# Optimization experiments

Measured on AMD Instinct MI355X. Metric: run time of the kernel, lower is better.

Reference implementation:

```python
import jax, jax.numpy as jnp
import numpy as np

N_NODES = 10000
N_EDGES = 640000
D_FEAT = 128
EPS = 1e-12  # F.normalize default eps


def setup_inputs() -> dict:
    key = jax.random.key(0)
    k1, k2, k3 = jax.random.split(key, 3)
    x = jax.random.normal(k1, (N_NODES, D_FEAT), dtype=jnp.float32)
    edge = jax.random.randint(k2, (3, N_EDGES), 0, N_NODES, dtype=jnp.int64)
    edge_weight = jax.random.uniform(k3, (N_EDGES,), dtype=jnp.float32)
    return {"x": x, "edge": edge, "edge_weight": edge_weight}


def reference(x, edge, edge_weight):
    edge_j = edge[0]  # source nodes
    edge_i = edge[2]  # target nodes
    n = x.shape[0]
    # degree of each target node (scatter_add of edge weights)
    deg = jax.ops.segment_sum(edge_weight, edge_i, num_segments=n)
    # normalized edge weights: w_e = ew_e / deg[target(e)]
    w = edge_weight / deg[edge_i]
    # SpMM: out[i] = sum_{e: target=i} w_e * x[source(e)]
    msg = x[edge_j] * w[:, None]           # [E, D]
    out = jax.ops.segment_sum(msg, edge_i, num_segments=n)  # [N, D]
    out = jax.nn.relu(out)
    # row-wise L2 normalize (F.normalize: x / max(||x||, eps))
    norm = jnp.sqrt(jnp.sum(out * out, axis=1, keepdims=True))
    return out / jnp.maximum(norm, EPS)
```

## Files before the change

kernel.cpp:

```cpp
#include <hip/hip_runtime.h>
#include <hip/hip_fp16.h>
#include <math.h>

#define D_FEAT 128
#define EPS 1e-12f
#define TGRP 40
#define NBUCK_PAD 256
#define NBLK 250
#define CAP_CB 40
#define SLOTS_PB (NBLK * CAP_CB)
#define LCAP 3584


__device__ inline float2 h2_to_f2(unsigned int u) {
    __half2 h = *reinterpret_cast<__half2*>(&u);
    return __half22float2(h);
}

__device__ inline float w12_to_f(unsigned int p) {
    return __half2float(__ushort_as_half((unsigned short)((p & 0xfffu) << 4)));
}

__global__ __launch_bounds__(1024)
void build_kernel(const int* __restrict__ edge_i,
                  const int* __restrict__ edge_j,
                  const float* __restrict__ ew,
                  const float* __restrict__ x,
                  unsigned int* __restrict__ xh,
                  unsigned char* __restrict__ cntcb,
                  unsigned int* __restrict__ payload,
                  int E, int total4, int nbuck) {
    __shared__ unsigned int hc[NBUCK_PAD];
    const int c   = blockIdx.x;
    const int tid = threadIdx.x;
    const int EPB = E / NBLK;

    if (tid < NBUCK_PAD) hc[tid] = 0;
    __syncthreads();

    for (int i = c * 1024 + tid; i < total4; i += NBLK * 1024) {
        float4 v = ((const float4*)x)[i];
        __half2 h01 = __floats2half2_rn(v.x, v.y);
        __half2 h23 = __floats2half2_rn(v.z, v.w);
        uint2 o;
        o.x = *reinterpret_cast<unsigned int*>(&h01);
        o.y = *reinterpret_cast<unsigned int*>(&h23);
        ((uint2*)xh)[i] = o;
    }

    const int e0 = c * EPB;
    for (int k = tid; k < EPB; k += 1024) {
        int e = e0 + k;
        int t = edge_i[e];
        int bkt  = t / TGRP;
        int tloc = t - bkt * TGRP;
        unsigned int r = atomicAdd(&hc[bkt], 1u);
        if (r < CAP_CB) {
            unsigned int hw = (unsigned int)__half_as_ushort(__float2half(ew[e]));
            unsigned int w12 = (hw + 8u) >> 4;
            payload[(size_t)bkt * SLOTS_PB + c * CAP_CB + r] =
                ((unsigned int)edge_j[e] << 18) | ((unsigned int)tloc << 12) | w12;
        }
    }
    __syncthreads();

    if (tid < nbuck) {
        unsigned int v = hc[tid];
        cntcb[(size_t)tid * NBUCK_PAD + c] =
            (unsigned char)(v > CAP_CB ? CAP_CB : v);
    }
}

__global__ __launch_bounds__(1024)
void sort_gather_kernel(const unsigned char* __restrict__ cntcb,
                        const unsigned int* __restrict__ payload,
                        const unsigned int* __restrict__ xh,
                        float* __restrict__ out, int n) {
    __shared__ unsigned char cnt_c[NBLK];
    __shared__ unsigned int  stmp[256];
    __shared__ unsigned int  chunkbase[NBLK + 1];
    __shared__ unsigned int  cnt40[TGRP];
    __shared__ unsigned int  base40[TGRP + 1];
    __shared__ unsigned int  ssw0[LCAP];
    __shared__ unsigned int  ssw[LCAP];
    const int b    = blockIdx.x;
    const int tid  = threadIdx.x;
    const int wv   = tid >> 6;
    const int lane = tid & 63;
    const int g    = lane >> 4;
    const int l16  = lane & 15;

    if (tid < NBLK) cnt_c[tid] = cntcb[(size_t)b * NBUCK_PAD + tid];
    if (tid < TGRP) cnt40[tid] = 0;
    __syncthreads();

    unsigned int v0 = 0;
    if (tid < 256) {
        v0 = (tid < NBLK) ? (unsigned int)cnt_c[tid] : 0u;
        stmp[tid] = v0;
    }
    __syncthreads();
    for (int off = 1; off < 256; off <<= 1) {
        unsigned int u = 0;
        if (tid < 256 && tid >= off) u = stmp[tid - off];
        __syncthreads();
        if (tid < 256) stmp[tid] += u;
        __syncthreads();
    }
    if (tid < NBLK) chunkbase[tid] = stmp[tid] - v0;
    if (tid == 255) chunkbase[NBLK] = stmp[255];
    __syncthreads();

    const unsigned int* __restrict__ pb = payload + (size_t)b * SLOTS_PB;
    for (int s = tid; s < SLOTS_PB; s += 1024) {
        unsigned int p = pb[s];
        int c = s / CAP_CB;
        int k = s - c * CAP_CB;
        if (k < (int)cnt_c[c]) {
            unsigned int pos = chunkbase[c] + (unsigned int)k;
            if (pos < LCAP) ssw0[pos] = p;
        }
    }
    __syncthreads();

    unsigned int M = chunkbase[NBLK];
    if (M > LCAP) M = LCAP;

    unsigned int pcar[4]; unsigned int dcar[4]; int ncar = 0;
    for (unsigned int i = tid; i < M; i += 1024) {
        unsigned int p = ssw0[i];
        unsigned int tloc = (p >> 12) & 63u;
        unsigned int r = atomicAdd(&cnt40[tloc], 1u);
        pcar[ncar] = p;
        dcar[ncar] = (tloc << 16) | (r & 0xffffu);
        ++ncar;
    }
    __syncthreads();

    if (tid == 0) {
        unsigned int run = 0;
        #pragma unroll
        for (int t = 0; t < TGRP; ++t) { base40[t] = run; run += cnt40[t]; }
        base40[TGRP] = run;
    }
    __syncthreads();

    for (int q = 0; q < ncar; ++q) {
        unsigned int d = dcar[q];
        unsigned int pos = base40[d >> 16] + (d & 0xffffu);
        if (pos < LCAP) ssw[pos] = pcar[q];
    }
    __syncthreads();

    const uint4* __restrict__ xr = (const uint4*)xh;
    for (int tl = wv; tl < TGRP; tl += 16) {
        int t = b * TGRP + tl;
        if (t >= n) break;
        int beg = (int)base40[tl];
        int m   = (int)cnt40[tl];
        if (beg + m > (int)LCAP) m = (LCAP - beg > 0) ? (LCAP - beg) : 0;

        float4 accA = {0.f,0.f,0.f,0.f};
        float4 accB = {0.f,0.f,0.f,0.f};

        int it = 0;
        for (; it + 15 < m; it += 16) {
            unsigned int pq[4]; uint4 hq[4];
            #pragma unroll
            for (int q = 0; q < 4; ++q) pq[q] = ssw[beg + it + q * 4 + g];
            #pragma unroll
            for (int q = 0; q < 4; ++q) hq[q] = xr[(size_t)(pq[q] >> 18) * 16 + l16];
            #pragma unroll
            for (int q = 0; q < 4; ++q) {
                float w = w12_to_f(pq[q]);
                float2 f;
                f = h2_to_f2(hq[q].x); accA.x = fmaf(f.x, w, accA.x); accA.y = fmaf(f.y, w, accA.y);
                f = h2_to_f2(hq[q].y); accA.z = fmaf(f.x, w, accA.z); accA.w = fmaf(f.y, w, accA.w);
                f = h2_to_f2(hq[q].z); accB.x = fmaf(f.x, w, accB.x); accB.y = fmaf(f.y, w, accB.y);
                f = h2_to_f2(hq[q].w); accB.z = fmaf(f.x, w, accB.z); accB.w = fmaf(f.y, w, accB.w);
            }
        }
        for (; it < m; it += 4) {
            int idx = it + g;
            unsigned int p = (idx < m) ? ssw[beg + idx] : 0u;
            uint4 h = xr[(size_t)(p >> 18) * 16 + l16];
            float w = w12_to_f(p);
            float2 f;
            f = h2_to_f2(h.x); accA.x = fmaf(f.x, w, accA.x); accA.y = fmaf(f.y, w, accA.y);
            f = h2_to_f2(h.y); accA.z = fmaf(f.x, w, accA.z); accA.w = fmaf(f.y, w, accA.w);
            f = h2_to_f2(h.z); accB.x = fmaf(f.x, w, accB.x); accB.y = fmaf(f.y, w, accB.y);
            f = h2_to_f2(h.w); accB.z = fmaf(f.x, w, accB.z); accB.w = fmaf(f.y, w, accB.w);
        }

        #pragma unroll
        for (int off = 16; off <= 32; off <<= 1) {
            accA.x += __shfl_xor(accA.x, off, 64);
            accA.y += __shfl_xor(accA.y, off, 64);
            accA.z += __shfl_xor(accA.z, off, 64);
            accA.w += __shfl_xor(accA.w, off, 64);
            accB.x += __shfl_xor(accB.x, off, 64);
            accB.y += __shfl_xor(accB.y, off, 64);
            accB.z += __shfl_xor(accB.z, off, 64);
            accB.w += __shfl_xor(accB.w, off, 64);
        }

        accA.x = fmaxf(accA.x, 0.f); accA.y = fmaxf(accA.y, 0.f);
        accA.z = fmaxf(accA.z, 0.f); accA.w = fmaxf(accA.w, 0.f);
        accB.x = fmaxf(accB.x, 0.f); accB.y = fmaxf(accB.y, 0.f);
        accB.z = fmaxf(accB.z, 0.f); accB.w = fmaxf(accB.w, 0.f);

        float ss = accA.x*accA.x + accA.y*accA.y + accA.z*accA.z + accA.w*accA.w
                 + accB.x*accB.x + accB.y*accB.y + accB.z*accB.z + accB.w*accB.w;
        #pragma unroll
        for (int off = 8; off > 0; off >>= 1) ss += __shfl_xor(ss, off, 64);

        float scale = 1.0f / fmaxf(sqrtf(ss), EPS);

        if (g == 0) {
            float4 o0 = { accA.x * scale, accA.y * scale, accA.z * scale, accA.w * scale };
            float4 o1 = { accB.x * scale, accB.y * scale, accB.z * scale, accB.w * scale };
            float4* orow = (float4*)out + (size_t)t * 32;
            orow[l16 * 2]     = o0;
            orow[l16 * 2 + 1] = o1;
        }
    }
}

__global__ void deg_kernel(const int* __restrict__ edge_i,
                           const float* __restrict__ ew,
                           float* __restrict__ deg, int E) {
    int e = blockIdx.x * blockDim.x + threadIdx.x;
    if (e < E) atomicAdd(&deg[edge_i[e]], ew[e]);
}

__global__ void scatter_kernel(const int* __restrict__ edge_j,
                               const int* __restrict__ edge_i,
                               const float* __restrict__ ew,
                               const float* __restrict__ deg,
                               const float* __restrict__ x,
                               float* __restrict__ out, int E) {
    int wave = (int)((blockIdx.x * (unsigned)blockDim.x + threadIdx.x) >> 6);
    int lane = threadIdx.x & 63;
    if (wave >= E) return;
    int tgt = edge_i[wave];
    int src = edge_j[wave];
    float w = ew[wave] / deg[tgt];
    const float2* xr = (const float2*)(x + (size_t)src * D_FEAT);
    float2 v = xr[lane];
    float* o = out + (size_t)tgt * D_FEAT + lane * 2;
    atomicAdd(o,     v.x * w);
    atomicAdd(o + 1, v.y * w);
}

__global__ void norm_kernel(float* __restrict__ out, int n) {
    int row = (int)((blockIdx.x * (unsigned)blockDim.x + threadIdx.x) >> 6);
    int lane = threadIdx.x & 63;
    if (row >= n) return;
    float2* o = (float2*)(out + (size_t)row * D_FEAT);
    float2 v = o[lane];
    v.x = fmaxf(v.x, 0.0f);
    v.y = fmaxf(v.y, 0.0f);
    float ss = v.x * v.x + v.y * v.y;
    #pragma unroll
    for (int off = 32; off > 0; off >>= 1) ss += __shfl_xor(ss, off, 64);
    float scale = 1.0f / fmaxf(sqrtf(ss), EPS);
    v.x *= scale;
    v.y *= scale;
    o[lane] = v;
}

static inline size_t align64(size_t v) { return (v + 63) & ~(size_t)63; }

extern "C" void kernel_launch(void* const* d_in, const int* in_sizes, int n_in,
                              void* d_out, int out_size, void* d_ws, size_t ws_size,
                              hipStream_t stream) {
    const float* x    = (const float*)d_in[0];
    const int*   edge = (const int*)d_in[1];
    const float* ew   = (const float*)d_in[2];
    float*       out  = (float*)d_out;

    const int E = in_sizes[2];
    const int n = in_sizes[0] / D_FEAT;

    const int* edge_j = edge;
    const int* edge_i = edge + 2 * (size_t)E;

    const int nbuck = (n + TGRP - 1) / TGRP;

    const size_t off_cnt = align64((size_t)n * D_FEAT * 2);
    const size_t off_pl  = align64(off_cnt + (size_t)nbuck * NBUCK_PAD);
    const size_t need    = off_pl + (size_t)nbuck * SLOTS_PB * 4;

    if (ws_size >= need && (E % NBLK) == 0 && nbuck <= NBLK &&
        (size_t)nbuck * TGRP >= (size_t)n && nbuck <= NBUCK_PAD && n <= 16384) {
        char* ws = (char*)d_ws;
        unsigned int*  xh      = (unsigned int*)ws;
        unsigned char* cntcb   = (unsigned char*)(ws + off_cnt);
        unsigned int*  payload = (unsigned int*)(ws + off_pl);

        const int total4 = n * D_FEAT / 4;

        build_kernel<<<NBLK, 1024, 0, stream>>>(edge_i, edge_j, ew, x, xh,
                                                cntcb, payload, E, total4, nbuck);
        sort_gather_kernel<<<nbuck, 1024, 0, stream>>>(cntcb, payload, xh,
                                                       out, n);
    } else {
        float* deg = (float*)d_ws;
        hipMemsetAsync(deg, 0, (size_t)n * sizeof(float), stream);
        hipMemsetAsync(out, 0, (size_t)out_size * sizeof(float), stream);
        deg_kernel<<<(E + 255) / 256, 256, 0, stream>>>(edge_i, ew, deg, E);
        scatter_kernel<<<(E + 3) / 4, 256, 0, stream>>>(edge_j, edge_i, ew, deg, x, out, E);
        norm_kernel<<<(n + 3) / 4, 256, 0, stream>>>(out, n);
    }
}
```

Before: 87.63 us.

## Fuse build and sort-gather kernels into one cooperative launch with grid sync

Merges the bucket-build phase and the sort/gather/normalize phase into a single cooperative kernel separated by a grid-wide barrier, with the original two-kernel path kept as a fallback if the cooperative launch fails. The aim is to remove the kernel launch boundary and inter-kernel gap between the two phases. In exchange, the fused kernel carries the shared-memory footprint of both phases, and a grid sync across 250 blocks of 1024 threads requires all of them to be co-resident, which can limit occupancy or fail the launch.

```diff
diff --git a/kernel.cpp b/kernel.cpp
--- a/kernel.cpp
+++ b/kernel.cpp
@@ -1,6 +1,9 @@
 #include <hip/hip_runtime.h>
 #include <hip/hip_fp16.h>
+#include <hip/hip_cooperative_groups.h>
 #include <math.h>
+
+namespace cg = cooperative_groups;
 
 #define D_FEAT 128
 #define EPS 1e-12f
@@ -21,20 +24,16 @@
     return __half2float(__ushort_as_half((unsigned short)((p & 0xfffu) << 4)));
 }
 
-__global__ __launch_bounds__(1024)
-void build_kernel(const int* __restrict__ edge_i,
-                  const int* __restrict__ edge_j,
-                  const float* __restrict__ ew,
-                  const float* __restrict__ x,
-                  unsigned int* __restrict__ xh,
-                  unsigned char* __restrict__ cntcb,
-                  unsigned int* __restrict__ payload,
-                  int E, int total4, int nbuck) {
-    __shared__ unsigned int hc[NBUCK_PAD];
-    const int c   = blockIdx.x;
-    const int tid = threadIdx.x;
-    const int EPB = E / NBLK;
-
+__device__ __forceinline__
+void phase1_impl(const int* __restrict__ edge_i,
+                 const int* __restrict__ edge_j,
+                 const float* __restrict__ ew,
+                 const float* __restrict__ x,
+                 unsigned int* __restrict__ xh,
+                 unsigned char* __restrict__ cntcb,
+                 unsigned int* __restrict__ payload,
+                 int E, int total4, int nbuck,
+                 int c, int tid, unsigned int* hc) {
     if (tid < NBUCK_PAD) hc[tid] = 0;
     __syncthreads();
 
@@ -48,6 +47,7 @@
         ((uint2*)xh)[i] = o;
     }
 
+    const int EPB = E / NBLK;
     const int e0 = c * EPB;
     for (int k = tid; k < EPB; k += 1024) {
         int e = e0 + k;
@@ -71,20 +71,16 @@
     }
 }
 
-__global__ __launch_bounds__(1024)
-void sort_gather_kernel(const unsigned char* __restrict__ cntcb,
-                        const unsigned int* __restrict__ payload,
-                        const unsigned int* __restrict__ xh,
-                        float* __restrict__ out, int n) {
-    __shared__ unsigned char cnt_c[NBLK];
-    __shared__ unsigned int  stmp[256];
-    __shared__ unsigned int  chunkbase[NBLK + 1];
-    __shared__ unsigned int  cnt40[TGRP];
-    __shared__ unsigned int  base40[TGRP + 1];
-    __shared__ unsigned int  ssw0[LCAP];
-    __shared__ unsigned int  ssw[LCAP];
-    const int b    = blockIdx.x;
-    const int tid  = threadIdx.x;
+__device__ __forceinline__
+void phase2_impl(const unsigned char* __restrict__ cntcb,
+                 const unsigned int* __restrict__ payload,
+                 const unsigned int* __restrict__ xh,
+                 float* __restrict__ out, int n,
+                 int b, int tid,
+                 unsigned char* cnt_c, unsigned int* stmp,
+                 unsigned int* chunkbase, unsigned int* cnt40,
+                 unsigned int* base40, unsigned int* ssw0,
+                 unsigned int* ssw) {
     const int wv   = tid >> 6;
     const int lane = tid & 63;
     const int g    = lane >> 4;
@@ -224,6 +220,70 @@
             orow[l16 * 2 + 1] = o1;
         }
     }
+}
+
+__global__ __launch_bounds__(1024)
+void fused_kernel(const int* __restrict__ edge_i,
+                  const int* __restrict__ edge_j,
+                  const float* __restrict__ ew,
+                  const float* __restrict__ x,
+                  unsigned int* __restrict__ xh,
+                  unsigned char* __restrict__ cntcb,
+                  unsigned int* __restrict__ payload,
+                  float* __restrict__ out,
+                  int E, int total4, int n, int nbuck) {
+    __shared__ unsigned int  hc[NBUCK_PAD];
+    __shared__ unsigned char cnt_c[NBLK];
+    __shared__ unsigned int  stmp[256];
+    __shared__ unsigned int  chunkbase[NBLK + 1];
+    __shared__ unsigned int  cnt40[TGRP];
+    __shared__ unsigned int  base40[TGRP + 1];
+    __shared__ unsigned int  ssw0[LCAP];
+    __shared__ unsigned int  ssw[LCAP];
+
+    const int bid = blockIdx.x;
+    const int tid = threadIdx.x;
+
+    phase1_impl(edge_i, edge_j, ew, x, xh, cntcb, payload,
+                E, total4, nbuck, bid, tid, hc);
+
+    __threadfence();
+    cg::this_grid().sync();
+
+    if (bid < nbuck) {
+        phase2_impl(cntcb, payload, xh, out, n, bid, tid,
+                    cnt_c, stmp, chunkbase, cnt40, base40, ssw0, ssw);
+    }
+}
+
+__global__ __launch_bounds__(1024)
+void build_kernel(const int* __restrict__ edge_i,
+                  const int* __restrict__ edge_j,
+                  const float* __restrict__ ew,
+                  const float* __restrict__ x,
+                  unsigned int* __restrict__ xh,
+                  unsigned char* __restrict__ cntcb,
+                  unsigned int* __restrict__ payload,
+                  int E, int total4, int nbuck) {
+    __shared__ unsigned int hc[NBUCK_PAD];
+    phase1_impl(edge_i, edge_j, ew, x, xh, cntcb, payload,
+                E, total4, nbuck, blockIdx.x, threadIdx.x, hc);
+}
+
+__global__ __launch_bounds__(1024)
+void sort_gather_kernel(const unsigned char* __restrict__ cntcb,
+                        const unsigned int* __restrict__ payload,
+                        const unsigned int* __restrict__ xh,
+                        float* __restrict__ out, int n) {
+    __shared__ unsigned char cnt_c[NBLK];
+    __shared__ unsigned int  stmp[256];
+    __shared__ unsigned int  chunkbase[NBLK + 1];
+    __shared__ unsigned int  cnt40[TGRP];
+    __shared__ unsigned int  base40[TGRP + 1];
+    __shared__ unsigned int  ssw0[LCAP];
+    __shared__ unsigned int  ssw[LCAP];
+    phase2_impl(cntcb, payload, xh, out, n, blockIdx.x, threadIdx.x,
+                cnt_c, stmp, chunkbase, cnt40, base40, ssw0, ssw);
 }
 
 __global__ void deg_kernel(const int* __restrict__ edge_i,
@@ -279,13 +339,13 @@
     const float* ew   = (const float*)d_in[2];
     float*       out  = (float*)d_out;
 
-    const int E = in_sizes[2];
-    const int n = in_sizes[0] / D_FEAT;
+    int E = in_sizes[2];
+    int n = in_sizes[0] / D_FEAT;
 
     const int* edge_j = edge;
     const int* edge_i = edge + 2 * (size_t)E;
 
-    const int nbuck = (n + TGRP - 1) / TGRP;
+    int nbuck = (n + TGRP - 1) / TGRP;
 
     const size_t off_cnt = align64((size_t)n * D_FEAT * 2);
     const size_t off_pl  = align64(off_cnt + (size_t)nbuck * NBUCK_PAD);
@@ -298,12 +358,24 @@
         unsigned char* cntcb   = (unsigned char*)(ws + off_cnt);
         unsigned int*  payload = (unsigned int*)(ws + off_pl);
 
-        const int total4 = n * D_FEAT / 4;
-
-        build_kernel<<<NBLK, 1024, 0, stream>>>(edge_i, edge_j, ew, x, xh,
-                                                cntcb, payload, E, total4, nbuck);
-        sort_gather_kernel<<<nbuck, 1024, 0, stream>>>(cntcb, payload, xh,
-                                                       out, n);
+        int total4 = n * D_FEAT / 4;
+
+        void* args[] = {
+            (void*)&edge_i, (void*)&edge_j, (void*)&ew, (void*)&x,
+            (void*)&xh, (void*)&cntcb, (void*)&payload, (void*)&out,
+            (void*)&E, (void*)&total4, (void*)&n, (void*)&nbuck
+        };
+        hipError_t err = hipLaunchCooperativeKernel((const void*)fused_kernel,
+                                                    dim3(NBLK), dim3(1024),
+                                                    args, 0, stream);
+        if (err != hipSuccess) {
+            (void)hipGetLastError();
+            build_kernel<<<NBLK, 1024, 0, stream>>>(edge_i, edge_j, ew, x, xh,
+                                                    cntcb, payload, E, total4,
+                                                    nbuck);
+            sort_gather_kernel<<<nbuck, 1024, 0, stream>>>(cntcb, payload, xh,
+                                                           out, n);
+        }
     } else {
         float* deg = (float*)d_ws;
         hipMemsetAsync(deg, 0, (size_t)n * sizeof(float), stream);
```

After: 211.3 us. 2.41x slower.
